# Kernel tuning notes

Measured on AMD Instinct MI355X. Metric: run time of the kernel, lower is better.

## Reference

```python
import jax, jax.numpy as jnp
import numpy as np

I = 1739   # input/output feature size (num_nodes)
H = 256    # hidden size
T = 2048   # trajectory length


def gru(x_seq, h0, W_ih, W_hh, b_ih, b_hh):
    """PyTorch-convention GRU over x_seq [T, I] with h0 [H]. Returns (hs [T,H], h_T [H])."""
    x_proj = x_seq @ W_ih.T + b_ih  # [T, 3H], precompute input projections

    def step(h, xp):
        hh = h @ W_hh.T + b_hh  # [3H]
        xr, xz, xn = xp[:H], xp[H:2 * H], xp[2 * H:]
        hr, hz, hn = hh[:H], hh[H:2 * H], hh[2 * H:]
        r = jax.nn.sigmoid(xr + hr)
        z = jax.nn.sigmoid(xz + hz)
        n = jnp.tanh(xn + r * hn)
        h_new = (1.0 - z) * n + z * h
        return h_new, h_new

    h_T, hs = jax.lax.scan(step, h0, x_proj)
    return hs, h_T


def setup_inputs() -> dict:
    key = jax.random.key(0)
    ks = jax.random.split(key, 12)
    s = 1.0 / np.sqrt(H)
    inp = {
        "input_trajectory": jax.random.normal(ks[0], (1, T, I), jnp.float32),
        "target_trajectory": jax.random.normal(ks[1], (1, T, I), jnp.float32),
        "W_ih_enc": jax.random.uniform(ks[2], (3 * H, I), jnp.float32, -s, s),
        "W_hh_enc": jax.random.uniform(ks[3], (3 * H, H), jnp.float32, -s, s),
        "b_ih_enc": jax.random.uniform(ks[4], (3 * H,), jnp.float32, -s, s),
        "b_hh_enc": jax.random.uniform(ks[5], (3 * H,), jnp.float32, -s, s),
        "W_ih_dec": jax.random.uniform(ks[6], (3 * H, I), jnp.float32, -s, s),
        "W_hh_dec": jax.random.uniform(ks[7], (3 * H, H), jnp.float32, -s, s),
        "b_ih_dec": jax.random.uniform(ks[8], (3 * H,), jnp.float32, -s, s),
        "b_hh_dec": jax.random.uniform(ks[9], (3 * H,), jnp.float32, -s, s),
        "W_out": jax.random.uniform(ks[10], (I, H), jnp.float32, -s, s),
        "b_out": jax.random.uniform(ks[11], (I,), jnp.float32, -s, s),
    }
    return inp


def reference(input_trajectory, target_trajectory,
              W_ih_enc, W_hh_enc, b_ih_enc, b_hh_enc,
              W_ih_dec, W_hh_dec, b_ih_dec, b_hh_dec,
              W_out, b_out):
    x = input_trajectory[0]  # [T, I], batch=1
    h0 = jnp.zeros((H,), x.dtype)
    # Encoder: only the final hidden state is used.
    _, h_enc = gru(x, h0, W_ih_enc, W_hh_enc, b_ih_enc, b_hh_enc)
    # Decoder: loop feeds each input timestep through a 1-step GRU;
    # this is exactly a GRU over the full sequence starting from h_enc.
    hs, _ = gru(x, h_enc, W_ih_dec, W_hh_dec, b_ih_dec, b_hh_dec)  # [T, H]
    # Per-step Linear is a single batched matmul over all steps.
    preds = hs @ W_out.T + b_out  # [T, I]
    # Original cats per-step (1,1,I) tensors along dim=0 -> [T, 1, I].
    return preds[:, None, :]
```

## Files before the change

kernel.cpp:

```cpp
#include <hip/hip_runtime.h>
#include <hip/hip_fp16.h>

#define TT 2048
#define II 1739
#define HN 256
#define H3 768
#define L2E 1.44269504088896f

typedef _Float16 h2 __attribute__((ext_vector_type(2)));

__device__ __forceinline__ float fdot2(h2 a, h2 b, float c) {
#if defined(__has_builtin)
#if __has_builtin(__builtin_amdgcn_fdot2)
  return __builtin_amdgcn_fdot2(a, b, c, false);
#else
  return fmaf((float)a[0], (float)b[0], fmaf((float)a[1], (float)b[1], c));
#endif
#else
  return fmaf((float)a[0], (float)b[0], fmaf((float)a[1], (float)b[1], c));
#endif
}

__device__ __forceinline__ float fast_exp2(float x) {
#if defined(__has_builtin)
#if __has_builtin(__builtin_amdgcn_exp2f)
  return __builtin_amdgcn_exp2f(x);
#else
  return exp2f(x);
#endif
#else
  return exp2f(x);
#endif
}

__device__ __forceinline__ float fast_rcp(float x) {
#if defined(__has_builtin)
#if __has_builtin(__builtin_amdgcn_rcpf)
  return __builtin_amdgcn_rcpf(x);
#else
  return 1.f / x;
#endif
#else
  return 1.f / x;
#endif
}

template <int CTRL>
__device__ __forceinline__ float dpp_qperm(float v) {
  int r = __builtin_amdgcn_update_dpp(0, __builtin_bit_cast(int, v), CTRL, 0xF, 0xF, true);
  return __builtin_bit_cast(float, r);
}

__global__ __launch_bounds__(256) void gemm_abt(
    const float* __restrict__ A, int M, int K,
    const float* __restrict__ B, int N,
    const float* __restrict__ bias1, const float* __restrict__ bias2, int b2lim,
    float s_lo, float s_hi, int slim,
    float* __restrict__ C) {
  __shared__ float As[16][64];
  __shared__ float Bs[16][64];
  const int tid = threadIdx.x;
  const int m0 = blockIdx.y * 64, n0 = blockIdx.x * 64;
  const int lr = tid >> 2;
  const int lk = (tid & 3) * 4;
  const int cx = tid & 15, cy = tid >> 4;
  float acc[4][4] = {};

  for (int k0 = 0; k0 < K; k0 += 16) {
#pragma unroll
    for (int i = 0; i < 4; ++i) {
      int k = k0 + lk + i;
      As[lk + i][lr] = (k < K) ? A[(size_t)(m0 + lr) * K + k] : 0.f;
      int bn = n0 + lr;
      Bs[lk + i][lr] = (k < K && bn < N) ? B[(size_t)bn * K + k] : 0.f;
    }
    __syncthreads();
#pragma unroll
    for (int k = 0; k < 16; ++k) {
      float4 av = *(const float4*)&As[k][cy * 4];
      float4 bv = *(const float4*)&Bs[k][cx * 4];
      const float aa[4] = {av.x, av.y, av.z, av.w};
      const float bb[4] = {bv.x, bv.y, bv.z, bv.w};
#pragma unroll
      for (int i = 0; i < 4; ++i)
#pragma unroll
        for (int j = 0; j < 4; ++j) acc[i][j] = fmaf(aa[i], bb[j], acc[i][j]);
    }
    __syncthreads();
  }
#pragma unroll
  for (int i = 0; i < 4; ++i) {
    int m = m0 + cy * 4 + i;
#pragma unroll
    for (int j = 0; j < 4; ++j) {
      int n = n0 + cx * 4 + j;
      if (n < N) {
        float b = bias1 ? bias1[n] : 0.f;
        if (bias2 && n < b2lim) b += bias2[n];
        float s = (n < slim) ? s_lo : s_hi;
        C[(size_t)m * N + n] = (acc[i][j] + b) * s;
      }
    }
  }
}

__global__ __launch_bounds__(512) void gru_seq(
    const float* __restrict__ xp,
    const float* __restrict__ Whh,
    const float* __restrict__ bhh,
    const float* __restrict__ h0,
    float* __restrict__ hs_out,
    float* __restrict__ hT_out) {
  __shared__ __align__(16) uint hbufd[2][160];

  const int tid = threadIdx.x;
  const int lane = tid & 63;
  const int wv = tid >> 6;
  const int kc = lane & 3;
  const int q = wv * 16 + (lane >> 2);
  const int u0 = 2 * q;

  h2 wreg[6][32];
#pragma unroll
  for (int uu = 0; uu < 2; ++uu) {
#pragma unroll
    for (int gg = 0; gg < 3; ++gg) {
      const float sc = (gg == 2) ? (2.f * L2E) : L2E;
      const float* wr = Whh + (size_t)(u0 + uu + gg * HN) * HN + kc * 64;
#pragma unroll
      for (int p = 0; p < 32; ++p) {
        float2 f = *(const float2*)(wr + 2 * p);
        wreg[uu * 3 + gg][p] = h2{(_Float16)(f.x * sc), (_Float16)(f.y * sc)};
      }
    }
  }

  float hj0 = h0 ? h0[u0] : 0.f;
  float hj1 = h0 ? h0[u0 + 1] : 0.f;
  const float bhn0 = bhh[2 * HN + u0] * (2.f * L2E);
  const float bhn1 = bhh[2 * HN + u0 + 1] * (2.f * L2E);

  if (tid < 128) {
    float a = h0 ? h0[2 * tid] : 0.f;
    float b = h0 ? h0[2 * tid + 1] : 0.f;
    h2 pv = h2{(_Float16)a, (_Float16)b};
    hbufd[0][(tid >> 5) * 40 + (tid & 31)] = __builtin_bit_cast(uint, pv);
  }
  __syncthreads();

  const float* xpt = xp + u0;
  const int wadr = (q >> 5) * 40 + (q & 31);

  for (int t = 0; t < TT; ++t) {
    float2 xr = *(const float2*)(xpt);
    float2 xz = *(const float2*)(xpt + HN);
    float2 xn = *(const float2*)(xpt + 2 * HN);
    xpt += H3;

    const uint* hb = &hbufd[t & 1][kc * 40];
    float a[6] = {0.f, 0.f, 0.f, 0.f, 0.f, 0.f};
#pragma unroll
    for (int qq = 0; qq < 8; ++qq) {
      uint4 v = *(const uint4*)&hb[qq * 4];
      uint hwv[4] = {v.x, v.y, v.z, v.w};
#pragma unroll
      for (int i = 0; i < 6; ++i)
#pragma unroll
        for (int p = 0; p < 4; ++p)
          a[i] = fdot2(wreg[i][qq * 4 + p], __builtin_bit_cast(h2, hwv[p]), a[i]);
    }

#pragma unroll
    for (int i = 0; i < 6; ++i) {
      float v = a[i];
      v += dpp_qperm<0xB1>(v);
      v += dpp_qperm<0x4E>(v);
      a[i] = v;
    }

    float r0 = fast_rcp(1.f + fast_exp2(-(xr.x + a[0])));
    float z0 = fast_rcp(1.f + fast_exp2(-(xz.x + a[1])));
    float n0 = fmaf(2.f, fast_rcp(1.f + fast_exp2(-fmaf(r0, a[2] + bhn0, xn.x))), -1.f);
    hj0 = fmaf(z0, hj0 - n0, n0);
    float r1 = fast_rcp(1.f + fast_exp2(-(xr.y + a[3])));
    float z1 = fast_rcp(1.f + fast_exp2(-(xz.y + a[4])));
    float n1 = fmaf(2.f, fast_rcp(1.f + fast_exp2(-fmaf(r1, a[5] + bhn1, xn.y))), -1.f);
    hj1 = fmaf(z1, hj1 - n1, n1);

    h2 pv = h2{(_Float16)hj0, (_Float16)hj1};
    if (kc == 0) {
      hbufd[(t & 1) ^ 1][wadr] = __builtin_bit_cast(uint, pv);
      if (hs_out) *(float2*)&hs_out[(size_t)t * HN + u0] = make_float2(hj0, hj1);
    }
    __syncthreads();
  }
  if (hT_out && kc == 0) *(float2*)&hT_out[u0] = make_float2(hj0, hj1);
}

extern "C" void kernel_launch(void* const* d_in, const int* in_sizes, int n_in,
                              void* d_out, int out_size, void* d_ws, size_t ws_size,
                              hipStream_t stream) {
  const float* x     = (const float*)d_in[0];
  const float* Wih_e = (const float*)d_in[2];
  const float* Whh_e = (const float*)d_in[3];
  const float* bih_e = (const float*)d_in[4];
  const float* bhh_e = (const float*)d_in[5];
  const float* Wih_d = (const float*)d_in[6];
  const float* Whh_d = (const float*)d_in[7];
  const float* bih_d = (const float*)d_in[8];
  const float* bhh_d = (const float*)d_in[9];
  const float* Wout  = (const float*)d_in[10];
  const float* bout  = (const float*)d_in[11];
  float* out = (float*)d_out;

  float* ws = (float*)d_ws;
  float* xpe  = ws;
  float* xpd  = xpe + (size_t)TT * H3;
  float* hs   = xpd + (size_t)TT * H3;
  float* henc = hs + (size_t)TT * HN;

  dim3 blk(256);
  gemm_abt<<<dim3(12, 32), blk, 0, stream>>>(x, TT, II, Wih_e, H3, bih_e, bhh_e, 2 * HN,
                                             L2E, 2.f * L2E, 2 * HN, xpe);
  gemm_abt<<<dim3(12, 32), blk, 0, stream>>>(x, TT, II, Wih_d, H3, bih_d, bhh_d, 2 * HN,
                                             L2E, 2.f * L2E, 2 * HN, xpd);
  gru_seq<<<1, 512, 0, stream>>>(xpe, Whh_e, bhh_e, nullptr, nullptr, henc);
  gru_seq<<<1, 512, 0, stream>>>(xpd, Whh_d, bhh_d, henc, hs, nullptr);
  gemm_abt<<<dim3(28, 32), blk, 0, stream>>>(hs, TT, HN, Wout, II, bout, nullptr, 0,
                                             1.f, 1.f, 0, out);
}
```

Baseline: 5.026 ms.

## Compute GRU recurrent matvec with MFMA f16 instructions instead of fdot2

Replaces the per-lane packed fp16 dot-product recurrence with 16x16x32 f16 MFMA instructions. Each wave holds its 32 hidden units' Whh rows for all three gates as A fragments in registers, and feeds the broadcast hidden state in as the B operand. The MFMA results go through a small per-wave LDS scratch so 32 lanes can each compute the gate nonlinearities for one hidden unit. This removes the DPP cross-lane reductions and the long fdot2 chains. In exchange it adds MFMA latency chains and an extra LDS write/read on every step, and 15 of every 16 output columns are redundant work.

```diff
diff --git a/kernel.cpp b/kernel.cpp
--- a/kernel.cpp
+++ b/kernel.cpp
@@ -7,19 +7,8 @@
 #define H3 768
 #define L2E 1.44269504088896f
 
-typedef _Float16 h2 __attribute__((ext_vector_type(2)));
-
-__device__ __forceinline__ float fdot2(h2 a, h2 b, float c) {
-#if defined(__has_builtin)
-#if __has_builtin(__builtin_amdgcn_fdot2)
-  return __builtin_amdgcn_fdot2(a, b, c, false);
-#else
-  return fmaf((float)a[0], (float)b[0], fmaf((float)a[1], (float)b[1], c));
-#endif
-#else
-  return fmaf((float)a[0], (float)b[0], fmaf((float)a[1], (float)b[1], c));
-#endif
-}
+typedef _Float16 h8 __attribute__((ext_vector_type(8)));
+typedef float f4 __attribute__((ext_vector_type(4)));
 
 __device__ __forceinline__ float fast_exp2(float x) {
 #if defined(__has_builtin)
@@ -43,12 +32,6 @@
 #else
   return 1.f / x;
 #endif
-}
-
-template <int CTRL>
-__device__ __forceinline__ float dpp_qperm(float v) {
-  int r = __builtin_amdgcn_update_dpp(0, __builtin_bit_cast(int, v), CTRL, 0xF, 0xF, true);
-  return __builtin_bit_cast(float, r);
 }
 
 __global__ __launch_bounds__(256) void gemm_abt(
@@ -104,97 +87,104 @@
   }
 }
 
-__global__ __launch_bounds__(512) void gru_seq(
+__global__ __attribute__((amdgpu_flat_work_group_size(512, 512)))
+__attribute__((amdgpu_waves_per_eu(2, 2))) void gru_seq(
     const float* __restrict__ xp,
     const float* __restrict__ Whh,
     const float* __restrict__ bhh,
     const float* __restrict__ h0,
     float* __restrict__ hs_out,
     float* __restrict__ hT_out) {
-  __shared__ __align__(16) uint hbufd[2][160];
+  __shared__ __align__(16) _Float16 hbuf[2][HN];
+  __shared__ __align__(16) float gsc[8][100];
 
   const int tid = threadIdx.x;
   const int lane = tid & 63;
   const int wv = tid >> 6;
-  const int kc = lane & 3;
-  const int q = wv * 16 + (lane >> 2);
-  const int u0 = 2 * q;
-
-  h2 wreg[6][32];
-#pragma unroll
-  for (int uu = 0; uu < 2; ++uu) {
-#pragma unroll
-    for (int gg = 0; gg < 3; ++gg) {
-      const float sc = (gg == 2) ? (2.f * L2E) : L2E;
-      const float* wr = Whh + (size_t)(u0 + uu + gg * HN) * HN + kc * 64;
-#pragma unroll
-      for (int p = 0; p < 32; ++p) {
-        float2 f = *(const float2*)(wr + 2 * p);
-        wreg[uu * 3 + gg][p] = h2{(_Float16)(f.x * sc), (_Float16)(f.y * sc)};
+  const int col = lane & 15;
+  const int kg = lane >> 4;
+  const int u = wv * 32 + lane;
+
+  h8 wfrag[6][8];
+#pragma unroll
+  for (int g = 0; g < 3; ++g) {
+#pragma unroll
+    for (int hf = 0; hf < 2; ++hf) {
+      const float sc = (g == 2) ? (2.f * L2E) : L2E;
+      const int row = g * HN + wv * 32 + hf * 16 + col;
+      const float* wr = Whh + (size_t)row * HN + kg * 8;
+#pragma unroll
+      for (int kk = 0; kk < 8; ++kk) {
+        float4 f0 = *(const float4*)(wr + kk * 32);
+        float4 f1 = *(const float4*)(wr + kk * 32 + 4);
+        h8 v;
+        v[0] = (_Float16)(f0.x * sc); v[1] = (_Float16)(f0.y * sc);
+        v[2] = (_Float16)(f0.z * sc); v[3] = (_Float16)(f0.w * sc);
+        v[4] = (_Float16)(f1.x * sc); v[5] = (_Float16)(f1.y * sc);
+        v[6] = (_Float16)(f1.z * sc); v[7] = (_Float16)(f1.w * sc);
+        wfrag[g * 2 + hf][kk] = v;
       }
     }
   }
 
-  float hj0 = h0 ? h0[u0] : 0.f;
-  float hj1 = h0 ? h0[u0 + 1] : 0.f;
-  const float bhn0 = bhh[2 * HN + u0] * (2.f * L2E);
-  const float bhn1 = bhh[2 * HN + u0 + 1] * (2.f * L2E);
-
-  if (tid < 128) {
-    float a = h0 ? h0[2 * tid] : 0.f;
-    float b = h0 ? h0[2 * tid + 1] : 0.f;
-    h2 pv = h2{(_Float16)a, (_Float16)b};
-    hbufd[0][(tid >> 5) * 40 + (tid & 31)] = __builtin_bit_cast(uint, pv);
+  float hj = 0.f, bhn = 0.f;
+  if (lane < 32) {
+    hj = h0 ? h0[u] : 0.f;
+    bhn = bhh[2 * HN + u] * (2.f * L2E);
+    hbuf[0][u] = (_Float16)hj;
   }
   __syncthreads();
 
-  const float* xpt = xp + u0;
-  const int wadr = (q >> 5) * 40 + (q & 31);
+  float* gw = &gsc[wv][0];
+  const f4 zero4 = {0.f, 0.f, 0.f, 0.f};
 
   for (int t = 0; t < TT; ++t) {
-    float2 xr = *(const float2*)(xpt);
-    float2 xz = *(const float2*)(xpt + HN);
-    float2 xn = *(const float2*)(xpt + 2 * HN);
-    xpt += H3;
-
-    const uint* hb = &hbufd[t & 1][kc * 40];
-    float a[6] = {0.f, 0.f, 0.f, 0.f, 0.f, 0.f};
-#pragma unroll
-    for (int qq = 0; qq < 8; ++qq) {
-      uint4 v = *(const uint4*)&hb[qq * 4];
-      uint hwv[4] = {v.x, v.y, v.z, v.w};
-#pragma unroll
-      for (int i = 0; i < 6; ++i)
-#pragma unroll
-        for (int p = 0; p < 4; ++p)
-          a[i] = fdot2(wreg[i][qq * 4 + p], __builtin_bit_cast(h2, hwv[p]), a[i]);
-    }
-
-#pragma unroll
-    for (int i = 0; i < 6; ++i) {
-      float v = a[i];
-      v += dpp_qperm<0xB1>(v);
-      v += dpp_qperm<0x4E>(v);
-      a[i] = v;
-    }
-
-    float r0 = fast_rcp(1.f + fast_exp2(-(xr.x + a[0])));
-    float z0 = fast_rcp(1.f + fast_exp2(-(xz.x + a[1])));
-    float n0 = fmaf(2.f, fast_rcp(1.f + fast_exp2(-fmaf(r0, a[2] + bhn0, xn.x))), -1.f);
-    hj0 = fmaf(z0, hj0 - n0, n0);
-    float r1 = fast_rcp(1.f + fast_exp2(-(xr.y + a[3])));
-    float z1 = fast_rcp(1.f + fast_exp2(-(xz.y + a[4])));
-    float n1 = fmaf(2.f, fast_rcp(1.f + fast_exp2(-fmaf(r1, a[5] + bhn1, xn.y))), -1.f);
-    hj1 = fmaf(z1, hj1 - n1, n1);
-
-    h2 pv = h2{(_Float16)hj0, (_Float16)hj1};
-    if (kc == 0) {
-      hbufd[(t & 1) ^ 1][wadr] = __builtin_bit_cast(uint, pv);
-      if (hs_out) *(float2*)&hs_out[(size_t)t * HN + u0] = make_float2(hj0, hj1);
+    float xr = 0.f, xz = 0.f, xn = 0.f;
+    if (lane < 32) {
+      const float* xpt = xp + (size_t)t * H3 + u;
+      xr = xpt[0];
+      xz = xpt[HN];
+      xn = xpt[2 * HN];
+    }
+
+    const _Float16* hc = &hbuf[t & 1][0];
+    f4 acc[6];
+    {
+      h8 b = *(const h8*)&hc[kg * 8];
+#pragma unroll
+      for (int f = 0; f < 6; ++f)
+        acc[f] = __builtin_amdgcn_mfma_f32_16x16x32_f16(wfrag[f][0], b, zero4, 0, 0, 0);
+    }
+#pragma unroll
+    for (int kk = 1; kk < 8; ++kk) {
+      h8 b = *(const h8*)&hc[kk * 32 + kg * 8];
+#pragma unroll
+      for (int f = 0; f < 6; ++f)
+        acc[f] = __builtin_amdgcn_mfma_f32_16x16x32_f16(wfrag[f][kk], b, acc[f], 0, 0, 0);
+    }
+
+    if (col == 0) {
+#pragma unroll
+      for (int g = 0; g < 3; ++g)
+#pragma unroll
+        for (int hf = 0; hf < 2; ++hf)
+          *(f4*)&gw[g * 32 + hf * 16 + kg * 4] = acc[g * 2 + hf];
+    }
+
+    if (lane < 32) {
+      float ar = gw[lane];
+      float az = gw[32 + lane];
+      float an = gw[64 + lane];
+      float r = fast_rcp(1.f + fast_exp2(-(xr + ar)));
+      float z = fast_rcp(1.f + fast_exp2(-(xz + az)));
+      float nv = fmaf(2.f, fast_rcp(1.f + fast_exp2(-fmaf(r, an + bhn, xn))), -1.f);
+      hj = fmaf(z, hj - nv, nv);
+      hbuf[(t & 1) ^ 1][u] = (_Float16)hj;
+      if (hs_out) hs_out[(size_t)t * HN + u] = hj;
     }
     __syncthreads();
   }
-  if (hT_out && kc == 0) *(float2*)&hT_out[u0] = make_float2(hj0, hj1);
+  if (hT_out && lane < 32) hT_out[u] = hj;
 }
 
 extern "C" void kernel_launch(void* const* d_in, const int* in_sizes, int n_in,
```

Measured after the change: 5.830 ms. 16.0% more time.

## Split GRU recurrence over 1024 threads, one hidden unit per lane group

Applied to the files above, without the earlier changes.

The sequential GRU kernel now runs with 1024 threads, so each 4-lane group owns one hidden unit instead of two. This halves the per-thread dot-product chain and the register-held weights on the per-step critical path. It also prefetches the next timestep's input projections before the current step's compute, hiding global-load latency. In exchange, the block-wide barrier now spans twice as many waves, and the new-h writes become 16-bit LDS stores from two lanes into the same word.

```diff
diff --git a/kernel.cpp b/kernel.cpp
--- a/kernel.cpp
+++ b/kernel.cpp
@@ -104,7 +104,8 @@
   }
 }
 
-__global__ __launch_bounds__(512) void gru_seq(
+__global__ __attribute__((amdgpu_flat_work_group_size(1024, 1024)))
+__attribute__((amdgpu_waves_per_eu(4, 4))) void gru_seq(
     const float* __restrict__ xp,
     const float* __restrict__ Whh,
     const float* __restrict__ bhh,
@@ -118,27 +119,21 @@
   const int wv = tid >> 6;
   const int kc = lane & 3;
   const int q = wv * 16 + (lane >> 2);
-  const int u0 = 2 * q;
-
-  h2 wreg[6][32];
-#pragma unroll
-  for (int uu = 0; uu < 2; ++uu) {
-#pragma unroll
-    for (int gg = 0; gg < 3; ++gg) {
-      const float sc = (gg == 2) ? (2.f * L2E) : L2E;
-      const float* wr = Whh + (size_t)(u0 + uu + gg * HN) * HN + kc * 64;
-#pragma unroll
-      for (int p = 0; p < 32; ++p) {
-        float2 f = *(const float2*)(wr + 2 * p);
-        wreg[uu * 3 + gg][p] = h2{(_Float16)(f.x * sc), (_Float16)(f.y * sc)};
-      }
-    }
-  }
-
-  float hj0 = h0 ? h0[u0] : 0.f;
-  float hj1 = h0 ? h0[u0 + 1] : 0.f;
-  const float bhn0 = bhh[2 * HN + u0] * (2.f * L2E);
-  const float bhn1 = bhh[2 * HN + u0 + 1] * (2.f * L2E);
+
+  h2 wreg[3][32];
+#pragma unroll
+  for (int gg = 0; gg < 3; ++gg) {
+    const float sc = (gg == 2) ? (2.f * L2E) : L2E;
+    const float* wr = Whh + (size_t)(gg * HN + q) * HN + kc * 64;
+#pragma unroll
+    for (int p = 0; p < 32; ++p) {
+      float2 f = *(const float2*)(wr + 2 * p);
+      wreg[gg][p] = h2{(_Float16)(f.x * sc), (_Float16)(f.y * sc)};
+    }
+  }
+
+  float hj = h0 ? h0[q] : 0.f;
+  const float bhn = bhh[2 * HN + q] * (2.f * L2E);
 
   if (tid < 128) {
     float a = h0 ? h0[2 * tid] : 0.f;
@@ -148,53 +143,52 @@
   }
   __syncthreads();
 
-  const float* xpt = xp + u0;
-  const int wadr = (q >> 5) * 40 + (q & 31);
+  _Float16* hwr0 = (_Float16*)&hbufd[0][(q >> 6) * 40 + ((q & 63) >> 1)];
+  _Float16* hwr1 = (_Float16*)&hbufd[1][(q >> 6) * 40 + ((q & 63) >> 1)];
+  const int hlo = q & 1;
+
+  const float* xq = xp + q;
+  float xr = xq[0], xz = xq[HN], xn = xq[2 * HN];
 
   for (int t = 0; t < TT; ++t) {
-    float2 xr = *(const float2*)(xpt);
-    float2 xz = *(const float2*)(xpt + HN);
-    float2 xn = *(const float2*)(xpt + 2 * HN);
-    xpt += H3;
+    const float* xqn = xq + (size_t)(t + 1) * H3;
+    float xr_n = xqn[0];
+    float xz_n = xqn[HN];
+    float xn_n = xqn[2 * HN];
 
     const uint* hb = &hbufd[t & 1][kc * 40];
-    float a[6] = {0.f, 0.f, 0.f, 0.f, 0.f, 0.f};
+    float a0 = 0.f, a1 = 0.f, a2 = 0.f;
 #pragma unroll
     for (int qq = 0; qq < 8; ++qq) {
       uint4 v = *(const uint4*)&hb[qq * 4];
       uint hwv[4] = {v.x, v.y, v.z, v.w};
 #pragma unroll
-      for (int i = 0; i < 6; ++i)
-#pragma unroll
-        for (int p = 0; p < 4; ++p)
-          a[i] = fdot2(wreg[i][qq * 4 + p], __builtin_bit_cast(h2, hwv[p]), a[i]);
-    }
-
-#pragma unroll
-    for (int i = 0; i < 6; ++i) {
-      float v = a[i];
-      v += dpp_qperm<0xB1>(v);
-      v += dpp_qperm<0x4E>(v);
-      a[i] = v;
-    }
-
-    float r0 = fast_rcp(1.f + fast_exp2(-(xr.x + a[0])));
-    float z0 = fast_rcp(1.f + fast_exp2(-(xz.x + a[1])));
-    float n0 = fmaf(2.f, fast_rcp(1.f + fast_exp2(-fmaf(r0, a[2] + bhn0, xn.x))), -1.f);
-    hj0 = fmaf(z0, hj0 - n0, n0);
-    float r1 = fast_rcp(1.f + fast_exp2(-(xr.y + a[3])));
-    float z1 = fast_rcp(1.f + fast_exp2(-(xz.y + a[4])));
-    float n1 = fmaf(2.f, fast_rcp(1.f + fast_exp2(-fmaf(r1, a[5] + bhn1, xn.y))), -1.f);
-    hj1 = fmaf(z1, hj1 - n1, n1);
-
-    h2 pv = h2{(_Float16)hj0, (_Float16)hj1};
+      for (int p = 0; p < 4; ++p) {
+        h2 hp = __builtin_bit_cast(h2, hwv[p]);
+        a0 = fdot2(wreg[0][qq * 4 + p], hp, a0);
+        a1 = fdot2(wreg[1][qq * 4 + p], hp, a1);
+        a2 = fdot2(wreg[2][qq * 4 + p], hp, a2);
+      }
+    }
+
+    a0 += dpp_qperm<0xB1>(a0); a0 += dpp_qperm<0x4E>(a0);
+    a1 += dpp_qperm<0xB1>(a1); a1 += dpp_qperm<0x4E>(a1);
+    a2 += dpp_qperm<0xB1>(a2); a2 += dpp_qperm<0x4E>(a2);
+
+    float r = fast_rcp(1.f + fast_exp2(-(xr + a0)));
+    float z = fast_rcp(1.f + fast_exp2(-(xz + a1)));
+    float nv = fmaf(2.f, fast_rcp(1.f + fast_exp2(-fmaf(r, a2 + bhn, xn))), -1.f);
+    hj = fmaf(z, hj - nv, nv);
+
     if (kc == 0) {
-      hbufd[(t & 1) ^ 1][wadr] = __builtin_bit_cast(uint, pv);
-      if (hs_out) *(float2*)&hs_out[(size_t)t * HN + u0] = make_float2(hj0, hj1);
-    }
+      _Float16* hw = (t & 1) ? hwr0 : hwr1;
+      hw[hlo] = (_Float16)hj;
+      if (hs_out) hs_out[(size_t)t * HN + q] = hj;
+    }
+    xr = xr_n; xz = xz_n; xn = xn_n;
     __syncthreads();
   }
-  if (hT_out && kc == 0) *(float2*)&hT_out[u0] = make_float2(hj0, hj1);
+  if (hT_out && kc == 0) hT_out[q] = hj;
 }
 
 extern "C" void kernel_launch(void* const* d_in, const int* in_sizes, int n_in,
@@ -224,8 +218,8 @@
                                              L2E, 2.f * L2E, 2 * HN, xpe);
   gemm_abt<<<dim3(12, 32), blk, 0, stream>>>(x, TT, II, Wih_d, H3, bih_d, bhh_d, 2 * HN,
                                              L2E, 2.f * L2E, 2 * HN, xpd);
-  gru_seq<<<1, 512, 0, stream>>>(xpe, Whh_e, bhh_e, nullptr, nullptr, henc);
-  gru_seq<<<1, 512, 0, stream>>>(xpd, Whh_d, bhh_d, henc, hs, nullptr);
+  gru_seq<<<1, 1024, 0, stream>>>(xpe, Whh_e, bhh_e, nullptr, nullptr, henc);
+  gru_seq<<<1, 1024, 0, stream>>>(xpd, Whh_d, bhh_d, henc, hs, nullptr);
   gemm_abt<<<dim3(28, 32), blk, 0, stream>>>(hs, TT, HN, Wout, II, bout, nullptr, 0,
                                              1.f, 1.f, 0, out);
 }
```

Measured after the change: 5.278 ms. +5.0%, slower.

## Split GRU recurrent weights between registers and LDS to relieve register pressure

Applied to the files above, without the earlier changes.

The recurrent GRU kernel previously held all 6x32 packed fp16 weight pairs per thread in registers. Now the first 20 pairs stay in registers and the remaining 12 are stored in dynamic shared memory, about 148 KB, and read back as uint4 each timestep. The aim is to cut VGPR pressure and likely spills in the latency-bound sequential loop. In exchange it adds 18 LDS loads per thread per step and needs a large dynamic LDS allocation set through hipFuncSetAttribute.

```diff
diff --git a/kernel.cpp b/kernel.cpp
--- a/kernel.cpp
+++ b/kernel.cpp
@@ -111,7 +111,9 @@
     const float* __restrict__ h0,
     float* __restrict__ hs_out,
     float* __restrict__ hT_out) {
-  __shared__ __align__(16) uint hbufd[2][160];
+  extern __shared__ __align__(16) uint lds[];
+  uint* hlds = lds;
+  uint* wlds = lds + 320;
 
   const int tid = threadIdx.x;
   const int lane = tid & 63;
@@ -120,17 +122,31 @@
   const int q = wv * 16 + (lane >> 2);
   const int u0 = 2 * q;
 
-  h2 wreg[6][32];
+  uint* wl = wlds + wv * 4608 + lane * 4;
+
+  h2 wreg[6][20];
 #pragma unroll
   for (int uu = 0; uu < 2; ++uu) {
 #pragma unroll
     for (int gg = 0; gg < 3; ++gg) {
       const float sc = (gg == 2) ? (2.f * L2E) : L2E;
       const float* wr = Whh + (size_t)(u0 + uu + gg * HN) * HN + kc * 64;
-#pragma unroll
-      for (int p = 0; p < 32; ++p) {
+      const int i = uu * 3 + gg;
+#pragma unroll
+      for (int p = 0; p < 20; ++p) {
         float2 f = *(const float2*)(wr + 2 * p);
-        wreg[uu * 3 + gg][p] = h2{(_Float16)(f.x * sc), (_Float16)(f.y * sc)};
+        wreg[i][p] = h2{(_Float16)(f.x * sc), (_Float16)(f.y * sc)};
+      }
+#pragma unroll
+      for (int j = 0; j < 3; ++j) {
+        const float* wb = wr + 40 + 8 * j;
+        h2 p0 = h2{(_Float16)(wb[0] * sc), (_Float16)(wb[1] * sc)};
+        h2 p1 = h2{(_Float16)(wb[2] * sc), (_Float16)(wb[3] * sc)};
+        h2 p2 = h2{(_Float16)(wb[4] * sc), (_Float16)(wb[5] * sc)};
+        h2 p3 = h2{(_Float16)(wb[6] * sc), (_Float16)(wb[7] * sc)};
+        uint4 w4 = {__builtin_bit_cast(uint, p0), __builtin_bit_cast(uint, p1),
+                    __builtin_bit_cast(uint, p2), __builtin_bit_cast(uint, p3)};
+        *(uint4*)&wl[(i * 3 + j) * 256] = w4;
       }
     }
   }
@@ -144,30 +160,47 @@
     float a = h0 ? h0[2 * tid] : 0.f;
     float b = h0 ? h0[2 * tid + 1] : 0.f;
     h2 pv = h2{(_Float16)a, (_Float16)b};
-    hbufd[0][(tid >> 5) * 40 + (tid & 31)] = __builtin_bit_cast(uint, pv);
+    hlds[(tid >> 5) * 40 + (tid & 31)] = __builtin_bit_cast(uint, pv);
   }
   __syncthreads();
 
-  const float* xpt = xp + u0;
   const int wadr = (q >> 5) * 40 + (q & 31);
 
   for (int t = 0; t < TT; ++t) {
-    float2 xr = *(const float2*)(xpt);
-    float2 xz = *(const float2*)(xpt + HN);
-    float2 xn = *(const float2*)(xpt + 2 * HN);
-    xpt += H3;
-
-    const uint* hb = &hbufd[t & 1][kc * 40];
+    float2 xr, xz, xn;
+    {
+      const float* xpt = xp + (size_t)t * H3 + u0;
+      xr = *(const float2*)(xpt);
+      xz = *(const float2*)(xpt + HN);
+      xn = *(const float2*)(xpt + 2 * HN);
+    }
+
+    const uint* hb = &hlds[(t & 1) * 160 + kc * 40];
     float a[6] = {0.f, 0.f, 0.f, 0.f, 0.f, 0.f};
 #pragma unroll
-    for (int qq = 0; qq < 8; ++qq) {
+    for (int qq = 0; qq < 5; ++qq) {
       uint4 v = *(const uint4*)&hb[qq * 4];
-      uint hwv[4] = {v.x, v.y, v.z, v.w};
+      uint hv[4] = {v.x, v.y, v.z, v.w};
 #pragma unroll
       for (int i = 0; i < 6; ++i)
 #pragma unroll
         for (int p = 0; p < 4; ++p)
-          a[i] = fdot2(wreg[i][qq * 4 + p], __builtin_bit_cast(h2, hwv[p]), a[i]);
+          a[i] = fdot2(wreg[i][qq * 4 + p], __builtin_bit_cast(h2, hv[p]), a[i]);
+    }
+
+#pragma unroll
+    for (int j = 0; j < 3; ++j) {
+      uint4 v = *(const uint4*)&hb[20 + j * 4];
+      uint hv[4] = {v.x, v.y, v.z, v.w};
+#pragma unroll
+      for (int i = 0; i < 6; ++i) {
+        uint4 w4 = *(const uint4*)&wl[(i * 3 + j) * 256];
+        uint wv4[4] = {w4.x, w4.y, w4.z, w4.w};
+#pragma unroll
+        for (int p = 0; p < 4; ++p)
+          a[i] = fdot2(__builtin_bit_cast(h2, wv4[p]),
+                       __builtin_bit_cast(h2, hv[p]), a[i]);
+      }
     }
 
 #pragma unroll
@@ -189,13 +222,15 @@
 
     h2 pv = h2{(_Float16)hj0, (_Float16)hj1};
     if (kc == 0) {
-      hbufd[(t & 1) ^ 1][wadr] = __builtin_bit_cast(uint, pv);
+      hlds[((t & 1) ^ 1) * 160 + wadr] = __builtin_bit_cast(uint, pv);
       if (hs_out) *(float2*)&hs_out[(size_t)t * HN + u0] = make_float2(hj0, hj1);
     }
     __syncthreads();
   }
   if (hT_out && kc == 0) *(float2*)&hT_out[u0] = make_float2(hj0, hj1);
 }
+
+#define GRU_LDS_BYTES ((320 + 8 * 18 * 256) * 4)
 
 extern "C" void kernel_launch(void* const* d_in, const int* in_sizes, int n_in,
                               void* d_out, int out_size, void* d_ws, size_t ws_size,
@@ -219,13 +254,21 @@
   float* hs   = xpd + (size_t)TT * H3;
   float* henc = hs + (size_t)TT * HN;
 
+  static bool s_attr = false;
+  if (!s_attr) {
+    hipFuncSetAttribute((const void*)gru_seq,
+                        hipFuncAttributeMaxDynamicSharedMemorySize,
+                        GRU_LDS_BYTES);
+    s_attr = true;
+  }
+
   dim3 blk(256);
   gemm_abt<<<dim3(12, 32), blk, 0, stream>>>(x, TT, II, Wih_e, H3, bih_e, bhh_e, 2 * HN,
                                              L2E, 2.f * L2E, 2 * HN, xpe);
   gemm_abt<<<dim3(12, 32), blk, 0, stream>>>(x, TT, II, Wih_d, H3, bih_d, bhh_d, 2 * HN,
                                              L2E, 2.f * L2E, 2 * HN, xpd);
-  gru_seq<<<1, 512, 0, stream>>>(xpe, Whh_e, bhh_e, nullptr, nullptr, henc);
-  gru_seq<<<1, 512, 0, stream>>>(xpd, Whh_d, bhh_d, henc, hs, nullptr);
+  gru_seq<<<1, 512, GRU_LDS_BYTES, stream>>>(xpe, Whh_e, bhh_e, nullptr, nullptr, henc);
+  gru_seq<<<1, 512, GRU_LDS_BYTES, stream>>>(xpd, Whh_d, bhh_d, henc, hs, nullptr);
   gemm_abt<<<dim3(28, 32), blk, 0, stream>>>(hs, TT, HN, Wout, II, bout, nullptr, 0,
                                              1.f, 1.f, 0, out);
 }
```

After: 5.569 ms. +10.8%, slower.
